# Performance work log

Measured on AMD Instinct MI355X. Metric: run time of the kernel, lower is better.

Reference implementation:

```python
import jax, jax.numpy as jnp
import numpy as np

B, S, D, H = 2, 2048, 1024, 16
HD = D // H          # 64
NREF = HD // 2       # 32 Householder reflections
BLOCK = 128          # flex_attention block granularity
ROPE_BASE = 10000.0


def setup_inputs() -> dict:
    key = jax.random.key(0)
    ks = jax.random.split(key, 12)
    x = jax.random.normal(ks[0], (B, S, D), jnp.float32)
    # block-causal block mask (flex_attention block_mask analogue)
    nb = S // BLOCK
    bm = jnp.tril(jnp.ones((nb, nb), bool))
    mask = jnp.repeat(jnp.repeat(bm, BLOCK, axis=0), BLOCK, axis=1)  # [S,S]
    s = lambda fan: fan ** -0.5
    vs = jax.random.normal(ks[1], (NREF, HD), jnp.float32) * 0.02
    w_qkv = jax.random.normal(ks[2], (D, 3 * D), jnp.float32) * s(D)
    w_out = jax.random.normal(ks[3], (D, D), jnp.float32) * s(D)
    w_gate = jax.random.normal(ks[4], (D, D), jnp.float32) * s(D)
    b_gate = jnp.zeros((D,), jnp.float32)
    w_mlp_gate = jax.random.normal(ks[5], (D, 8 * D), jnp.float32) * s(D)
    b_mlp_gate = jnp.zeros((8 * D,), jnp.float32)
    w_mlp_out = jax.random.normal(ks[6], (4 * D, D), jnp.float32) * s(4 * D)
    b_mlp_out = jnp.zeros((D,), jnp.float32)
    return dict(x=x, mask=mask, grid_size=S, vs=vs, w_qkv=w_qkv, w_out=w_out,
                w_gate=w_gate, b_gate=b_gate, w_mlp_gate=w_mlp_gate,
                b_mlp_gate=b_mlp_gate, w_mlp_out=w_mlp_out, b_mlp_out=b_mlp_out)


def rmsnorm(x):
    return x * jax.lax.rsqrt(jnp.mean(x * x, axis=-1, keepdims=True) + 1e-6)


def householder_matrix(vs):
    # Q = prod_i (I - 2 v_i v_i^T / |v_i|^2), applied sequentially as in torch loop
    def body(Q, v):
        vn = jnp.sum(v * v) + 1e-8
        return Q - (2.0 / vn) * jnp.outer(v, v @ Q), None
    Q0 = jnp.eye(HD, dtype=vs.dtype)
    Q, _ = jax.lax.scan(body, Q0, vs)
    return Q


def rope_tables(seq_len, dtype):
    inv_freq = 1.0 / (ROPE_BASE ** (jnp.arange(0, HD, 2, dtype=jnp.float32) / HD))
    ang = jnp.arange(seq_len, dtype=jnp.float32)[:, None] * inv_freq  # [S, HD/2]
    ang = jnp.concatenate([ang, ang], axis=-1)                        # [S, HD]
    return jnp.cos(ang).astype(dtype), jnp.sin(ang).astype(dtype)


def rotate_half(x):
    x1, x2 = jnp.split(x, 2, axis=-1)
    return jnp.concatenate([-x2, x1], axis=-1)


def reference(x, mask, grid_size, vs, w_qkv, w_out, w_gate, b_gate,
              w_mlp_gate, b_mlp_gate, w_mlp_out, b_mlp_out):
    del grid_size  # positions derived from sequence length
    resid = x
    h = rmsnorm(x)
    qkv = h @ w_qkv                                # [B,S,3D]
    q, k, v = jnp.split(qkv, 3, axis=-1)
    to_heads = lambda t: t.reshape(B, S, H, HD).transpose(0, 2, 1, 3)  # [B,H,S,hd]
    q, k, v = to_heads(q), to_heads(k), to_heads(v)

    # RnRoPE: inverse Householder rotation, rope, forward Householder rotation
    Q = householder_matrix(vs)                     # [hd,hd]
    q = q @ Q.T
    k = k @ Q.T
    cos, sin = rope_tables(S, x.dtype)             # [S,hd]
    cos = cos[None, None]; sin = sin[None, None]
    q = q * cos + rotate_half(q) * sin
    k = k * cos + rotate_half(k) * sin
    q = q @ Q
    k = k @ Q

    # block-sparse attention (mask realized as boolean [S,S])
    scores = jnp.einsum('bhqd,bhkd->bhqk', q, k) / jnp.sqrt(jnp.asarray(HD, x.dtype))
    scores = jnp.where(mask[None, None], scores, jnp.asarray(-1e30, x.dtype))
    attn = jnp.einsum('bhqk,bhkd->bhqd', jax.nn.softmax(scores, axis=-1), v)
    attn = attn.transpose(0, 2, 1, 3).reshape(B, S, D)
    attn = attn @ w_out

    gate = jax.nn.sigmoid(attn @ w_gate + b_gate)
    x = resid + attn * gate

    resid = x
    gv = rmsnorm(x) @ w_mlp_gate + b_mlp_gate      # [B,S,8D]
    g, val = jnp.split(gv, 2, axis=-1)
    x = resid + (val * jax.nn.gelu(g, approximate=False)) @ w_mlp_out + b_mlp_out
    return x
```

## Files before the change

kernel.cpp:

```cpp
#include <hip/hip_runtime.h>
#include <hip/hip_bf16.h>
#include <math.h>

#define BT 2
#define SEQ 2048
#define DIM 1024
#define NH 16
#define HD 64
#define NTOK (BT*SEQ)

typedef __attribute__((ext_vector_type(4))) float floatx4;
typedef __attribute__((ext_vector_type(8))) short shortx8;
typedef __attribute__((ext_vector_type(4))) short shortx4;

#define GLL16(gp, lp) __builtin_amdgcn_global_load_lds( \
    (const __attribute__((address_space(1))) unsigned int*)(const void*)(gp), \
    (__attribute__((address_space(3))) unsigned int*)(void*)(lp), 16, 0, 0)

__device__ __forceinline__ float bf2f(unsigned short u) {
    unsigned int x = ((unsigned int)u) << 16;
    return __builtin_bit_cast(float, x);
}
__device__ __forceinline__ unsigned short f2bf(float f) {
    unsigned int x = __builtin_bit_cast(unsigned int, f);
    unsigned int lsb = (x >> 16) & 1u;
    x += 0x7fffu + lsb;
    return (unsigned short)(x >> 16);
}
__device__ __forceinline__ float ldin_f(const void* p, size_t i, int isbf) {
    return isbf ? bf2f(((const unsigned short*)p)[i]) : ((const float*)p)[i];
}

__global__ void detect_kernel(const unsigned short* __restrict__ x, int* __restrict__ flag) {
    __shared__ int cnt;
    if (threadIdx.x == 0) cnt = 0;
    __syncthreads();
    unsigned short u = x[(size_t)threadIdx.x * 2];
    int e = (u >> 7) & 0xFF;
    if (e >= 100 && e <= 140) atomicAdd(&cnt, 1);
    __syncthreads();
    if (threadIdx.x == 0) *flag = (cnt >= 192) ? 1 : 0;
}

__global__ void transpose_any(const void* __restrict__ in,
                              unsigned short* __restrict__ out, int R, int C,
                              const int* __restrict__ flagp) {
    int isbf = *flagp;
    __shared__ unsigned short tile[32][33];
    int c0 = blockIdx.x * 32, r0 = blockIdx.y * 32;
    int tx = threadIdx.x, ty = threadIdx.y;
#pragma unroll
    for (int i = 0; i < 4; i++) {
        size_t idx = (size_t)(r0 + ty + i * 8) * C + c0 + tx;
        tile[ty + i * 8][tx] = isbf ? ((const unsigned short*)in)[idx]
                                    : f2bf(((const float*)in)[idx]);
    }
    __syncthreads();
#pragma unroll
    for (int i = 0; i < 4; i++)
        out[(size_t)(c0 + ty + i * 8) * R + r0 + tx] = tile[tx][ty + i * 8];
}

__global__ __launch_bounds__(64) void householder_kernel(const void* __restrict__ vs,
                                                         float* __restrict__ Qg,
                                                         const int* __restrict__ flagp) {
    int isbf = *flagp;
    __shared__ float vsh[64];
    int j = threadIdx.x;
    float Qc[64];
#pragma unroll
    for (int i = 0; i < 64; i++) Qc[i] = (i == j) ? 1.f : 0.f;
    for (int r = 0; r < 32; r++) {
        vsh[j] = ldin_f(vs, r * 64 + j, isbf);
        __syncthreads();
        float va[64];
#pragma unroll
        for (int i = 0; i < 64; i++) va[i] = vsh[i];
        float vn0 = 0.f, vn1 = 0.f, vn2 = 0.f, vn3 = 0.f;
        float t0 = 0.f, t1 = 0.f, t2 = 0.f, t3 = 0.f;
#pragma unroll
        for (int i = 0; i < 16; i++) {
            vn0 += va[4 * i + 0] * va[4 * i + 0];
            vn1 += va[4 * i + 1] * va[4 * i + 1];
            vn2 += va[4 * i + 2] * va[4 * i + 2];
            vn3 += va[4 * i + 3] * va[4 * i + 3];
            t0 += va[4 * i + 0] * Qc[4 * i + 0];
            t1 += va[4 * i + 1] * Qc[4 * i + 1];
            t2 += va[4 * i + 2] * Qc[4 * i + 2];
            t3 += va[4 * i + 3] * Qc[4 * i + 3];
        }
        float vn = (vn0 + vn1) + (vn2 + vn3) + 1e-8f;
        float t = (t0 + t1) + (t2 + t3);
        float c = (2.f / vn) * t;
#pragma unroll
        for (int i = 0; i < 64; i++) Qc[i] -= c * va[i];
        __syncthreads();
    }
#pragma unroll
    for (int i = 0; i < 64; i++) Qg[i * 64 + j] = Qc[i];
}

__global__ __launch_bounds__(256) void rotate_wqkv(unsigned short* __restrict__ wT,
                                                   const float* __restrict__ Qg) {
    __shared__ float Qs[64][64];
    __shared__ unsigned short tile[64][128];
    int bid = blockIdx.x;
    int row0 = (bid >> 3) * 64;
    int col0 = (bid & 7) * 128;
    int t = threadIdx.x;
#pragma unroll
    for (int i = 0; i < 16; i++) {
        int idx = i * 256 + t;
        Qs[idx >> 6][idx & 63] = Qg[idx];
    }
#pragma unroll
    for (int i = 0; i < 8; i++) {
        int e = i * 256 + t;
        int r = e >> 5, cg = (e & 31) * 4;
        *(shortx4*)&tile[r][cg] = *(const shortx4*)&wT[(size_t)(row0 + r) * 1024 + col0 + cg];
    }
    __syncthreads();
    int ib = t >> 5;
    int c = (t & 31) * 4;
    float acc[8][4];
#pragma unroll
    for (int rr = 0; rr < 8; rr++)
#pragma unroll
        for (int cx = 0; cx < 4; cx++) acc[rr][cx] = 0.f;
    for (int j = 0; j < 64; j++) {
        float t0 = bf2f(tile[j][c]);
        float t1 = bf2f(tile[j][c + 1]);
        float t2 = bf2f(tile[j][c + 2]);
        float t3 = bf2f(tile[j][c + 3]);
#pragma unroll
        for (int rr = 0; rr < 8; rr++) {
            float qv = Qs[rr * 8 + ib][j];
            acc[rr][0] += qv * t0;
            acc[rr][1] += qv * t1;
            acc[rr][2] += qv * t2;
            acc[rr][3] += qv * t3;
        }
    }
#pragma unroll
    for (int rr = 0; rr < 8; rr++) {
        int i = rr * 8 + ib;
        shortx4 o4;
#pragma unroll
        for (int cx = 0; cx < 4; cx++) o4[cx] = (short)f2bf(acc[rr][cx]);
        *(shortx4*)&wT[(size_t)(row0 + i) * 1024 + col0 + c] = o4;
    }
}

__global__ void rope_table(float* __restrict__ tab) {
    int idx = blockIdx.x * 256 + threadIdx.x;
    int s = idx >> 5, fi = idx & 31;
    float invf = __expf(-(float)fi * (9.210340371976184f / 32.f));
    float ang = (float)s * invf;
    tab[2 * idx]     = cosf(ang);
    tab[2 * idx + 1] = sinf(ang);
}

__global__ __launch_bounds__(256) void rmsnorm2(const void* __restrict__ x,
                                                unsigned short* __restrict__ h,
                                                const int* __restrict__ flagp) {
    int isbf = flagp ? *flagp : 1;
    __shared__ float red[256];
    int row = blockIdx.x, t = threadIdx.x;
    size_t base = (size_t)row * DIM;
    float v[4];
    float ss = 0.f;
#pragma unroll
    for (int i = 0; i < 4; i++) {
        v[i] = ldin_f(x, base + t + 256 * i, isbf);
        ss += v[i] * v[i];
    }
    red[t] = ss;
    __syncthreads();
    for (int s = 128; s > 0; s >>= 1) {
        if (t < s) red[t] += red[t + s];
        __syncthreads();
    }
    float rs = rsqrtf(red[0] * (1.f / 1024.f) + 1e-6f);
#pragma unroll
    for (int i = 0; i < 4; i++) h[base + t + 256 * i] = f2bf(v[i] * rs);
}

#define GBM 128
#define GBN 128
#define GBK 32

__global__ __launch_bounds__(256) void gemm_bt(const unsigned short* __restrict__ A,
                                               const unsigned short* __restrict__ Bt,
                                               void* __restrict__ C,
                                               const void* __restrict__ bias,
                                               const unsigned short* __restrict__ resid,
                                               const int* __restrict__ flagp,
                                               int M, int N, int K, int c_f32) {
    __shared__ __align__(16) unsigned short As[GBM][GBK];
    __shared__ __align__(16) unsigned short Bs[GBN][GBK];
    int bisbf = (bias && flagp) ? *flagp : 1;
    int nbn = N / GBN;
    int m0 = (blockIdx.x / nbn) * GBM;
    int n0 = (blockIdx.x % nbn) * GBN;
    int t = threadIdx.x;
    int lane = t & 63;
    int w = t >> 6;
    int wr = (w >> 1) * 64;
    int wc = (w & 1) * 64;
    int lr = lane & 15;
    int kg = lane >> 4;

    floatx4 acc[4][4];
#pragma unroll
    for (int i = 0; i < 4; i++)
#pragma unroll
        for (int j = 0; j < 4; j++) acc[i][j] = (floatx4){0.f, 0.f, 0.f, 0.f};

    int srow = w * 16 + (lane >> 2);
    int skseg = (lane & 3) * 8;
    const unsigned short* aP = A + (size_t)(m0 + srow) * K + skseg;
    const unsigned short* bP = Bt + (size_t)(n0 + srow) * K + skseg;
    unsigned short* aL0 = &As[w * 16][0];
    unsigned short* aL1 = &As[64 + w * 16][0];
    unsigned short* bL0 = &Bs[w * 16][0];
    unsigned short* bL1 = &Bs[64 + w * 16][0];
    size_t r64 = (size_t)64 * K;

    for (int k0 = 0; k0 < K; k0 += GBK) {
        __syncthreads();
        GLL16(aP + k0,       aL0);
        GLL16(aP + r64 + k0, aL1);
        GLL16(bP + k0,       bL0);
        GLL16(bP + r64 + k0, bL1);
        __syncthreads();
        shortx8 af[4], bfv[4];
#pragma unroll
        for (int i = 0; i < 4; i++) af[i] = *(const shortx8*)&As[wr + i * 16 + lr][kg * 8];
#pragma unroll
        for (int j = 0; j < 4; j++) bfv[j] = *(const shortx8*)&Bs[wc + j * 16 + lr][kg * 8];
#pragma unroll
        for (int i = 0; i < 4; i++)
#pragma unroll
            for (int j = 0; j < 4; j++)
                acc[i][j] = __builtin_amdgcn_mfma_f32_16x16x32_bf16(af[i], bfv[j], acc[i][j], 0, 0, 0);
    }
#pragma unroll
    for (int i = 0; i < 4; i++) {
#pragma unroll
        for (int j = 0; j < 4; j++) {
            int col = n0 + wc + j * 16 + lr;
            int rbase = m0 + wr + i * 16 + kg * 4;
            float bv = bias ? ldin_f(bias, col, bisbf) : 0.f;
#pragma unroll
            for (int r = 0; r < 4; r++) {
                float val = acc[i][j][r] + bv;
                size_t oidx = (size_t)(rbase + r) * N + col;
                if (resid) val += bf2f(resid[oidx]);
                if (c_f32) ((float*)C)[oidx] = val;
                else       ((unsigned short*)C)[oidx] = f2bf(val);
            }
        }
    }
}

__global__ __launch_bounds__(256) void qk_rope3(const unsigned short* __restrict__ qkv,
                                                const float* __restrict__ tab,
                                                unsigned short* __restrict__ q_r,
                                                unsigned short* __restrict__ k_r) {
    int tid = blockIdx.x * 256 + threadIdx.x;
    int c = tid & 3;
    int h = (tid >> 2) & 15;
    int ts = tid >> 6;
    int s = ts & 2047, b = ts >> 11;
    int d0 = c * 8;
    const unsigned short* base = qkv + (size_t)ts * 3072 + h * 64;
    shortx8 qlo = *(const shortx8*)(base + d0);
    shortx8 qhi = *(const shortx8*)(base + d0 + 32);
    shortx8 klo = *(const shortx8*)(base + 1024 + d0);
    shortx8 khi = *(const shortx8*)(base + 1024 + d0 + 32);
    const float* tp = tab + (size_t)s * 64 + d0 * 2;
    shortx8 oql, oqh, okl, okh;
#pragma unroll
    for (int i = 0; i < 8; i++) {
        float cv = tp[2 * i], sv = tp[2 * i + 1];
        float ql = bf2f((unsigned short)qlo[i]), qh = bf2f((unsigned short)qhi[i]);
        float kl = bf2f((unsigned short)klo[i]), kh = bf2f((unsigned short)khi[i]);
        oql[i] = (short)f2bf(ql * cv - qh * sv);
        oqh[i] = (short)f2bf(qh * cv + ql * sv);
        okl[i] = (short)f2bf(kl * cv - kh * sv);
        okh[i] = (short)f2bf(kh * cv + kl * sv);
    }
    size_t o = ((size_t)(b * NH + h) * SEQ + s) * HD + d0;
    *(shortx8*)(q_r + o)      = oql;
    *(shortx8*)(q_r + o + 32) = oqh;
    *(shortx8*)(k_r + o)      = okl;
    *(shortx8*)(k_r + o + 32) = okh;
}

__global__ __launch_bounds__(512) void attn_mfma(const unsigned short* __restrict__ q_r,
                                                 const unsigned short* __restrict__ k_r,
                                                 const unsigned short* __restrict__ qkv,
                                                 unsigned short* __restrict__ attn) {
    __shared__ __align__(16) unsigned short Ks[64][72];
    __shared__ __align__(16) unsigned short Vt[64 * 72];
    __shared__ __align__(16) unsigned short Ps[8][16][72];
    int bid = blockIdx.x;
    int qblk = 15 - (bid & 15);
    int bh = bid >> 4;
    int b = bh >> 4, h = bh & 15;
    size_t bh_off = (size_t)bh * SEQ * HD;
    int tid = threadIdx.x;
    int wv = tid >> 6, lane = tid & 63;
    int l16 = lane & 15, quad = lane >> 4;
    int q0 = qblk * 128 + wv * 16;

    const unsigned short* qrow = q_r + bh_off + (size_t)(q0 + l16) * HD + quad * 8;
    shortx8 aq0 = *(const shortx8*)(qrow);
    shortx8 aq1 = *(const shortx8*)(qrow + 32);

    floatx4 o[4];
#pragma unroll
    for (int nt = 0; nt < 4; nt++) o[nt] = (floatx4){0.f, 0.f, 0.f, 0.f};
    float m4[4] = {-1e30f, -1e30f, -1e30f, -1e30f};
    float l4[4] = {0.f, 0.f, 0.f, 0.f};

    int nk = (qblk + 1) * 128;
    int skey = tid >> 3;
    int sd0 = (tid & 7) * 8;
    const unsigned short* kbase = k_r + bh_off + (size_t)skey * HD + sd0;
    const unsigned short* vbase = qkv + ((size_t)(b * SEQ + skey)) * 3072 + 2048 + h * 64 + sd0;
    int vco = (((skey >> 3) ^ (tid & 7)) * 8) + (skey & 7);

    shortx8 kv = *(const shortx8*)kbase;
    shortx8 vvv = *(const shortx8*)vbase;

    for (int k0 = 0; k0 < nk; k0 += 64) {
        __syncthreads();
        *(shortx8*)&Ks[skey][sd0] = kv;
#pragma unroll
        for (int i = 0; i < 8; i++) Vt[(size_t)(sd0 + i) * 72 + vco] = (unsigned short)vvv[i];
        __syncthreads();
        if (k0 + 64 < nk) {
            kv  = *(const shortx8*)(kbase + (size_t)(k0 + 64) * HD);
            vvv = *(const shortx8*)(vbase + (size_t)(k0 + 64) * 3072);
        }

        floatx4 sc[4];
#pragma unroll
        for (int kt = 0; kt < 4; kt++) {
            shortx8 bk0 = *(const shortx8*)&Ks[kt * 16 + l16][quad * 8];
            shortx8 bk1 = *(const shortx8*)&Ks[kt * 16 + l16][32 + quad * 8];
            floatx4 z = (floatx4){0.f, 0.f, 0.f, 0.f};
            z = __builtin_amdgcn_mfma_f32_16x16x32_bf16(aq0, bk0, z, 0, 0, 0);
            z = __builtin_amdgcn_mfma_f32_16x16x32_bf16(aq1, bk1, z, 0, 0, 0);
            sc[kt] = z;
        }
#pragma unroll
        for (int r = 0; r < 4; r++) {
            float s0 = sc[0][r] * 0.125f;
            float s1 = sc[1][r] * 0.125f;
            float s2 = sc[2][r] * 0.125f;
            float s3 = sc[3][r] * 0.125f;
            float mt = fmaxf(fmaxf(s0, s1), fmaxf(s2, s3));
#pragma unroll
            for (int msk = 1; msk < 16; msk <<= 1) mt = fmaxf(mt, __shfl_xor(mt, msk, 64));
            float nmr = fmaxf(m4[r], mt);
            float al = __expf(m4[r] - nmr);
            m4[r] = nmr;
            float p0 = __expf(s0 - nmr);
            float p1 = __expf(s1 - nmr);
            float p2 = __expf(s2 - nmr);
            float p3 = __expf(s3 - nmr);
            float ps = (p0 + p1) + (p2 + p3);
#pragma unroll
            for (int msk = 1; msk < 16; msk <<= 1) ps += __shfl_xor(ps, msk, 64);
            l4[r] = l4[r] * al + ps;
#pragma unroll
            for (int nt = 0; nt < 4; nt++) o[nt][r] *= al;
            int pr = quad * 4 + r;
            Ps[wv][pr][l16]      = f2bf(p0);
            Ps[wv][pr][16 + l16] = f2bf(p1);
            Ps[wv][pr][32 + l16] = f2bf(p2);
            Ps[wv][pr][48 + l16] = f2bf(p3);
        }
#pragma unroll
        for (int h2 = 0; h2 < 2; h2++) {
            shortx8 ap = *(const shortx8*)&Ps[wv][l16][h2 * 32 + quad * 8];
#pragma unroll
            for (int nt = 0; nt < 4; nt++) {
                int dd = nt * 16 + l16;
                shortx8 bvv = *(const shortx8*)&Vt[(size_t)dd * 72 +
                                                   (((h2 * 4 + quad) ^ ((dd >> 3) & 7)) * 8)];
                o[nt] = __builtin_amdgcn_mfma_f32_16x16x32_bf16(ap, bvv, o[nt], 0, 0, 0);
            }
        }
    }
#pragma unroll
    for (int r = 0; r < 4; r++) {
        float inv_l = 1.f / l4[r];
        int s = q0 + quad * 4 + r;
        unsigned short* op = attn + ((size_t)(b * SEQ + s)) * DIM + h * 64;
#pragma unroll
        for (int nt = 0; nt < 4; nt++) op[nt * 16 + l16] = f2bf(o[nt][r] * inv_l);
    }
}

__global__ void combine_gate(const void* __restrict__ x,
                             const unsigned short* __restrict__ ao,
                             const unsigned short* __restrict__ gl,
                             const void* __restrict__ bg,
                             unsigned short* __restrict__ x1,
                             const int* __restrict__ flagp) {
    int isbf = *flagp;
    size_t idx = (size_t)blockIdx.x * 256 + threadIdx.x;
    float a = bf2f(ao[idx]);
    float z = bf2f(gl[idx]) + ldin_f(bg, idx & 1023, isbf);
    float sg = 1.f / (1.f + __expf(-z));
    x1[idx] = f2bf(ldin_f(x, idx, isbf) + a * sg);
}

__global__ void glu_kernel(const unsigned short* __restrict__ gv,
                           unsigned short* __restrict__ act) {
    size_t idx = (size_t)blockIdx.x * 256 + threadIdx.x;
    size_t m = idx >> 12, n = idx & 4095;
    float g = bf2f(gv[m * 8192 + n]);
    float val = bf2f(gv[m * 8192 + 4096 + n]);
    float ge = 0.5f * g * (1.f + erff(g * 0.70710678118f));
    act[idx] = f2bf(val * ge);
}

extern "C" void kernel_launch(void* const* d_in, const int* in_sizes, int n_in,
                              void* d_out, int out_size, void* d_ws, size_t ws_size,
                              hipStream_t stream) {
    const unsigned short* x        = (const unsigned short*)d_in[0];
    const void* vs       = d_in[3];
    const void* w_qkv    = d_in[4];
    const void* w_out    = d_in[5];
    const void* w_gate   = d_in[6];
    const void* b_gate   = d_in[7];
    const void* w_mlp_g  = d_in[8];
    const void* b_mlp_g  = d_in[9];
    const void* w_mlp_o  = d_in[10];
    const void* b_mlp_o  = d_in[11];
    float* out = (float*)d_out;
    char* ws = (char*)d_ws;

    if (n_in < 12) return;
    if (in_sizes[0] != 4194304 || in_sizes[3] != 2048 || in_sizes[4] != 3145728 ||
        in_sizes[8] != 8388608 || in_sizes[10] != 4194304 || in_sizes[7] != 1024) return;

    const size_t o_T   = 0;
    const size_t o_Qg  = 35651584;
    const size_t o_h   = 35684352;
    const size_t o_B   = 44072960;
    const size_t o_C   = 69238784;
    const size_t o_gv  = 94404608;
    const size_t total = 161513472;
    if (ws_size < total) return;

    unsigned short* wqkvT  = (unsigned short*)(ws + o_T);
    unsigned short* woutT  = (unsigned short*)(ws + o_T + 6291456);
    unsigned short* wgateT = (unsigned short*)(ws + o_T + 8388608);
    unsigned short* wmgT   = (unsigned short*)(ws + o_T + 10485760);
    unsigned short* wmoT   = (unsigned short*)(ws + o_T + 27262976);
    float*          Qg     = (float*)(ws + o_Qg);
    int*            flagp  = (int*)(ws + o_Qg + 16384);
    unsigned short* h      = (unsigned short*)(ws + o_h);
    unsigned short* qkv    = (unsigned short*)(ws + o_B);
    unsigned short* ao     = (unsigned short*)(ws + o_B + 8388608);
    unsigned short* gl     = (unsigned short*)(ws + o_B + 16777216);
    unsigned short* q_rb   = (unsigned short*)(ws + o_C);
    unsigned short* k_rb   = (unsigned short*)(ws + o_C + 8388608);
    unsigned short* attnb  = (unsigned short*)(ws + o_C + 16777216);
    unsigned short* x1     = (unsigned short*)(ws + o_C);
    unsigned short* act    = (unsigned short*)(ws + o_C + 8388608);
    float*          rtab   = (float*)(ws + o_gv);
    unsigned short* gv     = (unsigned short*)(ws + o_gv);

    detect_kernel<<<1, 256, 0, stream>>>(x, flagp);
    householder_kernel<<<1, 64, 0, stream>>>(vs, Qg, flagp);
    rope_table<<<256, 256, 0, stream>>>(rtab);

    dim3 tb(32, 8);
    transpose_any<<<dim3(3072 / 32, 1024 / 32), tb, 0, stream>>>(w_qkv,   wqkvT, 1024, 3072, flagp);
    transpose_any<<<dim3(1024 / 32, 1024 / 32), tb, 0, stream>>>(w_out,   woutT, 1024, 1024, flagp);
    transpose_any<<<dim3(1024 / 32, 1024 / 32), tb, 0, stream>>>(w_gate,  wgateT, 1024, 1024, flagp);
    transpose_any<<<dim3(8192 / 32, 1024 / 32), tb, 0, stream>>>(w_mlp_g, wmgT, 1024, 8192, flagp);
    transpose_any<<<dim3(1024 / 32, 4096 / 32), tb, 0, stream>>>(w_mlp_o, wmoT, 4096, 1024, flagp);
    rotate_wqkv<<<256, 256, 0, stream>>>(wqkvT, Qg);

    rmsnorm2<<<NTOK, 256, 0, stream>>>(x, h, flagp);
    gemm_bt<<<32 * 24, 256, 0, stream>>>(h, wqkvT, qkv, nullptr, nullptr, flagp, NTOK, 3072, 1024, 0);
    qk_rope3<<<1024, 256, 0, stream>>>(qkv, rtab, q_rb, k_rb);
    attn_mfma<<<BT * NH * (SEQ / 128), 512, 0, stream>>>(q_rb, k_rb, qkv, attnb);
    gemm_bt<<<32 * 8, 256, 0, stream>>>(attnb, woutT, ao, nullptr, nullptr, flagp, NTOK, 1024, 1024, 0);
    gemm_bt<<<32 * 8, 256, 0, stream>>>(ao, wgateT, gl, nullptr, nullptr, flagp, NTOK, 1024, 1024, 0);
    combine_gate<<<NTOK * DIM / 256, 256, 0, stream>>>(x, ao, gl, b_gate, x1, flagp);
    rmsnorm2<<<NTOK, 256, 0, stream>>>(x1, h, nullptr);
    gemm_bt<<<32 * 64, 256, 0, stream>>>(h, wmgT, gv, b_mlp_g, nullptr, flagp, NTOK, 8192, 1024, 0);
    glu_kernel<<<NTOK * 4096 / 256, 256, 0, stream>>>(gv, act);
    gemm_bt<<<32 * 8, 256, 0, stream>>>(act, wmoT, (void*)out, b_mlp_o, x1, flagp, NTOK, 1024, 4096, 1);
}
```

Measured before the change: 672.4 us.

## Fuse GELU-GLU into MLP gate GEMM and transpose attention score layout

Adds a GEMM kernel that computes the gate and value halves of the MLP up-projection together and applies bias, exact GELU and the product in its epilogue. This removes the 8192-wide intermediate write and re-read and one launch. In attention, the QK MFMA operands are swapped so each lane holds one query row's scores, which replaces the per-row 16-lane shuffle reductions with in-register reductions plus two shuffles and allows vectorised P stores. The fused GEMM doubles the accumulator registers, which may reduce occupancy.

```diff
diff --git a/kernel.cpp b/kernel.cpp
--- a/kernel.cpp
+++ b/kernel.cpp
@@ -263,6 +263,91 @@
     }
 }
 
+__global__ __launch_bounds__(256) void gemm_glu(const unsigned short* __restrict__ A,
+                                                const unsigned short* __restrict__ Bt,
+                                                unsigned short* __restrict__ act,
+                                                const void* __restrict__ bias,
+                                                const int* __restrict__ flagp) {
+    __shared__ __align__(16) unsigned short As[128][32];
+    __shared__ __align__(16) unsigned short Bs1[128][32];
+    __shared__ __align__(16) unsigned short Bs2[128][32];
+    const int K = 1024;
+    int isbf = *flagp;
+    int m0 = (blockIdx.x >> 5) * 128;
+    int n0 = (blockIdx.x & 31) * 128;
+    int t = threadIdx.x;
+    int lane = t & 63;
+    int w = t >> 6;
+    int wr = (w >> 1) * 64;
+    int wc = (w & 1) * 64;
+    int lr = lane & 15;
+    int kg = lane >> 4;
+
+    floatx4 acc[4][4], acc2[4][4];
+#pragma unroll
+    for (int i = 0; i < 4; i++)
+#pragma unroll
+        for (int j = 0; j < 4; j++) {
+            acc[i][j] = (floatx4){0.f, 0.f, 0.f, 0.f};
+            acc2[i][j] = (floatx4){0.f, 0.f, 0.f, 0.f};
+        }
+
+    int srow = w * 16 + (lane >> 2);
+    int skseg = (lane & 3) * 8;
+    const unsigned short* aP  = A + (size_t)(m0 + srow) * K + skseg;
+    const unsigned short* b1P = Bt + (size_t)(n0 + srow) * K + skseg;
+    const unsigned short* b2P = Bt + (size_t)(4096 + n0 + srow) * K + skseg;
+    unsigned short* aL0 = &As[w * 16][0];
+    unsigned short* aL1 = &As[64 + w * 16][0];
+    unsigned short* c1L0 = &Bs1[w * 16][0];
+    unsigned short* c1L1 = &Bs1[64 + w * 16][0];
+    unsigned short* c2L0 = &Bs2[w * 16][0];
+    unsigned short* c2L1 = &Bs2[64 + w * 16][0];
+    size_t r64 = (size_t)64 * K;
+
+    for (int k0 = 0; k0 < K; k0 += 32) {
+        __syncthreads();
+        GLL16(aP + k0,        aL0);
+        GLL16(aP + r64 + k0,  aL1);
+        GLL16(b1P + k0,       c1L0);
+        GLL16(b1P + r64 + k0, c1L1);
+        GLL16(b2P + k0,       c2L0);
+        GLL16(b2P + r64 + k0, c2L1);
+        __syncthreads();
+        shortx8 af[4], bf1[4], bf2v[4];
+#pragma unroll
+        for (int i = 0; i < 4; i++) af[i]   = *(const shortx8*)&As[wr + i * 16 + lr][kg * 8];
+#pragma unroll
+        for (int j = 0; j < 4; j++) bf1[j]  = *(const shortx8*)&Bs1[wc + j * 16 + lr][kg * 8];
+#pragma unroll
+        for (int j = 0; j < 4; j++) bf2v[j] = *(const shortx8*)&Bs2[wc + j * 16 + lr][kg * 8];
+#pragma unroll
+        for (int i = 0; i < 4; i++)
+#pragma unroll
+            for (int j = 0; j < 4; j++) {
+                acc[i][j]  = __builtin_amdgcn_mfma_f32_16x16x32_bf16(af[i], bf1[j],  acc[i][j], 0, 0, 0);
+                acc2[i][j] = __builtin_amdgcn_mfma_f32_16x16x32_bf16(af[i], bf2v[j], acc2[i][j], 0, 0, 0);
+            }
+    }
+#pragma unroll
+    for (int i = 0; i < 4; i++) {
+#pragma unroll
+        for (int j = 0; j < 4; j++) {
+            int col = n0 + wc + j * 16 + lr;
+            int rbase = m0 + wr + i * 16 + kg * 4;
+            float bg = ldin_f(bias, col, isbf);
+            float bv = ldin_f(bias, 4096 + col, isbf);
+#pragma unroll
+            for (int r = 0; r < 4; r++) {
+                float g = acc[i][j][r] + bg;
+                float v = acc2[i][j][r] + bv;
+                float ge = 0.5f * g * (1.f + erff(g * 0.70710678118f));
+                act[(size_t)(rbase + r) * 4096 + col] = f2bf(v * ge);
+            }
+        }
+    }
+}
+
 __global__ __launch_bounds__(256) void qk_rope3(const unsigned short* __restrict__ qkv,
                                                 const float* __restrict__ tab,
                                                 unsigned short* __restrict__ q_r,
@@ -321,8 +406,7 @@
     floatx4 o[4];
 #pragma unroll
     for (int nt = 0; nt < 4; nt++) o[nt] = (floatx4){0.f, 0.f, 0.f, 0.f};
-    float m4[4] = {-1e30f, -1e30f, -1e30f, -1e30f};
-    float l4[4] = {0.f, 0.f, 0.f, 0.f};
+    float m_run = -1e30f, l_run = 0.f;
 
     int nk = (qblk + 1) * 128;
     int skey = tid >> 3;
@@ -351,37 +435,49 @@
             shortx8 bk0 = *(const shortx8*)&Ks[kt * 16 + l16][quad * 8];
             shortx8 bk1 = *(const shortx8*)&Ks[kt * 16 + l16][32 + quad * 8];
             floatx4 z = (floatx4){0.f, 0.f, 0.f, 0.f};
-            z = __builtin_amdgcn_mfma_f32_16x16x32_bf16(aq0, bk0, z, 0, 0, 0);
-            z = __builtin_amdgcn_mfma_f32_16x16x32_bf16(aq1, bk1, z, 0, 0, 0);
+            z = __builtin_amdgcn_mfma_f32_16x16x32_bf16(bk0, aq0, z, 0, 0, 0);
+            z = __builtin_amdgcn_mfma_f32_16x16x32_bf16(bk1, aq1, z, 0, 0, 0);
             sc[kt] = z;
         }
+        float sv[16], mx[16];
+#pragma unroll
+        for (int kt = 0; kt < 4; kt++)
+#pragma unroll
+            for (int r = 0; r < 4; r++) sv[kt * 4 + r] = sc[kt][r] * 0.125f;
+#pragma unroll
+        for (int i = 0; i < 16; i++) mx[i] = sv[i];
+#pragma unroll
+        for (int st = 8; st > 0; st >>= 1)
+#pragma unroll
+            for (int i = 0; i < 8; i++)
+                if (i < st) mx[i] = fmaxf(mx[i], mx[i + st]);
+        float mt = mx[0];
+        mt = fmaxf(mt, __shfl_xor(mt, 16, 64));
+        mt = fmaxf(mt, __shfl_xor(mt, 32, 64));
+        float nm = fmaxf(m_run, mt);
+        float al = __expf(m_run - nm);
+        m_run = nm;
+        float p[16];
+#pragma unroll
+        for (int i = 0; i < 16; i++) p[i] = __expf(sv[i] - nm);
+        float sm[8];
+#pragma unroll
+        for (int i = 0; i < 8; i++) sm[i] = p[i] + p[i + 8];
+        float ps = ((sm[0] + sm[1]) + (sm[2] + sm[3])) + ((sm[4] + sm[5]) + (sm[6] + sm[7]));
+        ps += __shfl_xor(ps, 16, 64);
+        ps += __shfl_xor(ps, 32, 64);
+        l_run = l_run * al + ps;
+#pragma unroll
+        for (int kt = 0; kt < 4; kt++) {
+            shortx4 pk;
+#pragma unroll
+            for (int r = 0; r < 4; r++) pk[r] = (short)f2bf(p[kt * 4 + r]);
+            *(shortx4*)&Ps[wv][l16][kt * 16 + quad * 4] = pk;
+        }
 #pragma unroll
         for (int r = 0; r < 4; r++) {
-            float s0 = sc[0][r] * 0.125f;
-            float s1 = sc[1][r] * 0.125f;
-            float s2 = sc[2][r] * 0.125f;
-            float s3 = sc[3][r] * 0.125f;
-            float mt = fmaxf(fmaxf(s0, s1), fmaxf(s2, s3));
-#pragma unroll
-            for (int msk = 1; msk < 16; msk <<= 1) mt = fmaxf(mt, __shfl_xor(mt, msk, 64));
-            float nmr = fmaxf(m4[r], mt);
-            float al = __expf(m4[r] - nmr);
-            m4[r] = nmr;
-            float p0 = __expf(s0 - nmr);
-            float p1 = __expf(s1 - nmr);
-            float p2 = __expf(s2 - nmr);
-            float p3 = __expf(s3 - nmr);
-            float ps = (p0 + p1) + (p2 + p3);
-#pragma unroll
-            for (int msk = 1; msk < 16; msk <<= 1) ps += __shfl_xor(ps, msk, 64);
-            l4[r] = l4[r] * al + ps;
-#pragma unroll
-            for (int nt = 0; nt < 4; nt++) o[nt][r] *= al;
-            int pr = quad * 4 + r;
-            Ps[wv][pr][l16]      = f2bf(p0);
-            Ps[wv][pr][16 + l16] = f2bf(p1);
-            Ps[wv][pr][32 + l16] = f2bf(p2);
-            Ps[wv][pr][48 + l16] = f2bf(p3);
+            float alr = __shfl(al, quad * 4 + r, 64);
+            o[0][r] *= alr; o[1][r] *= alr; o[2][r] *= alr; o[3][r] *= alr;
         }
 #pragma unroll
         for (int h2 = 0; h2 < 2; h2++) {
@@ -397,7 +493,8 @@
     }
 #pragma unroll
     for (int r = 0; r < 4; r++) {
-        float inv_l = 1.f / l4[r];
+        float lv = __shfl(l_run, quad * 4 + r, 64);
+        float inv_l = 1.f / lv;
         int s = q0 + quad * 4 + r;
         unsigned short* op = attn + ((size_t)(b * SEQ + s)) * DIM + h * 64;
 #pragma unroll
@@ -417,16 +514,6 @@
     float z = bf2f(gl[idx]) + ldin_f(bg, idx & 1023, isbf);
     float sg = 1.f / (1.f + __expf(-z));
     x1[idx] = f2bf(ldin_f(x, idx, isbf) + a * sg);
-}
-
-__global__ void glu_kernel(const unsigned short* __restrict__ gv,
-                           unsigned short* __restrict__ act) {
-    size_t idx = (size_t)blockIdx.x * 256 + threadIdx.x;
-    size_t m = idx >> 12, n = idx & 4095;
-    float g = bf2f(gv[m * 8192 + n]);
-    float val = bf2f(gv[m * 8192 + 4096 + n]);
-    float ge = 0.5f * g * (1.f + erff(g * 0.70710678118f));
-    act[idx] = f2bf(val * ge);
 }
 
 extern "C" void kernel_launch(void* const* d_in, const int* in_sizes, int n_in,
@@ -475,7 +562,6 @@
     unsigned short* x1     = (unsigned short*)(ws + o_C);
     unsigned short* act    = (unsigned short*)(ws + o_C + 8388608);
     float*          rtab   = (float*)(ws + o_gv);
-    unsigned short* gv     = (unsigned short*)(ws + o_gv);
 
     detect_kernel<<<1, 256, 0, stream>>>(x, flagp);
     householder_kernel<<<1, 64, 0, stream>>>(vs, Qg, flagp);
@@ -497,7 +583,6 @@
     gemm_bt<<<32 * 8, 256, 0, stream>>>(ao, wgateT, gl, nullptr, nullptr, flagp, NTOK, 1024, 1024, 0);
     combine_gate<<<NTOK * DIM / 256, 256, 0, stream>>>(x, ao, gl, b_gate, x1, flagp);
     rmsnorm2<<<NTOK, 256, 0, stream>>>(x1, h, nullptr);
-    gemm_bt<<<32 * 64, 256, 0, stream>>>(h, wmgT, gv, b_mlp_g, nullptr, flagp, NTOK, 8192, 1024, 0);
-    glu_kernel<<<NTOK * 4096 / 256, 256, 0, stream>>>(gv, act);
+    gemm_glu<<<32 * 32, 256, 0, stream>>>(h, wmgT, act, b_mlp_g, flagp);
     gemm_bt<<<32 * 8, 256, 0, stream>>>(act, wmoT, (void*)out, b_mlp_o, x1, flagp, NTOK, 1024, 4096, 1);
 }
```

After: 689.3 us. +2.5%, slower.
